# Kernel optimization log

Measured on AMD Instinct MI355X. Metric: run time of the kernel, lower is better.

## Reference

```python
import jax, jax.numpy as jnp
import numpy as np

B, S, D, H, HD = 1, 2048, 1024, 16, 64
WINDOW = 512
RADIUS = max(1, WINDOW // 2)
GLOBAL_IDX = (0, 1, 2, 3)
NEG = -1e9


def rotate_half(x):
    x1, x2 = jnp.split(x, 2, axis=-1)
    return jnp.concatenate([-x2, x1], axis=-1)


def apply_rope(x, cos, sin, pos):
    # x: [b, s, h, hd]; cos/sin: [max_pos, hd]; pos: [b, s]
    c = cos[pos][:, :, None, :]
    s_ = sin[pos][:, :, None, :]
    return x * c + rotate_half(x) * s_


def setup_inputs() -> dict:
    key = jax.random.key(0)
    ks = jax.random.split(key, 12)
    x = jax.random.normal(ks[0], (B, S, D), dtype=jnp.float32)
    # RoPE tables (standard construction)
    inv_freq = 1.0 / (10000.0 ** (jnp.arange(0, HD, 2, dtype=jnp.float32) / HD))
    t = jnp.arange(S, dtype=jnp.float32)
    freqs = jnp.outer(t, inv_freq)                      # [S, HD/2]
    emb = jnp.concatenate([freqs, freqs], axis=-1)      # [S, HD]
    cos_freqs = jnp.cos(emb)
    sin_freqs = jnp.sin(emb)
    position_ids = jnp.broadcast_to(jnp.arange(S, dtype=jnp.int32), (B, S))
    w = lambda k: jax.random.normal(k, (D, D), dtype=jnp.float32) * 0.02
    return {
        "x": x, "cos_freqs": cos_freqs, "sin_freqs": sin_freqs,
        "position_ids": position_ids,
        "Wqs": w(ks[1]), "Wks": w(ks[2]), "Wvs": w(ks[3]),
        "Wqg": w(ks[4]), "Wkg": w(ks[5]), "Wvg": w(ks[6]),
        "Wo": w(ks[7]),
    }


def reference(x, cos_freqs, sin_freqs, position_ids, Wqs, Wks, Wvs, Wqg, Wkg, Wvg, Wo):
    b, s, d = x.shape
    split = lambda y: y.reshape(b, s, H, HD)
    qs = split(x @ Wqs)
    ks_ = split(x @ Wks)
    vs = split(x @ Wvs)
    kg = split(x @ Wkg)
    vg = split(x @ Wvg)
    # (qg projection exists in the module but is unused by its forward math)
    qs = apply_rope(qs, cos_freqs, sin_freqs, position_ids)
    ks_ = apply_rope(ks_, cos_freqs, sin_freqs, position_ids)

    qs_t = jnp.swapaxes(qs, 1, 2)   # [b,h,s,hd]
    ks_t = jnp.swapaxes(ks_, 1, 2)
    vs_t = jnp.swapaxes(vs, 1, 2)
    scale = 1.0 / jnp.sqrt(jnp.float32(HD))

    # local sliding-window (causal) attention over dense scores
    scores = jnp.einsum('bhsd,bhtd->bhst', qs_t, ks_t) * scale
    i = jnp.arange(s)[:, None]
    j = jnp.arange(s)[None, :]
    mask = (jnp.abs(i - j) <= RADIUS) & (j <= i)
    scores = jnp.where(mask[None, None], scores, NEG)
    g = jnp.array(GLOBAL_IDX)
    scores = scores.at[:, :, :, g].add(1e9)  # same as per-index set(score+1e9)
    attn = jax.nn.softmax(scores, axis=-1)
    out_local = jnp.einsum('bhst,bhtd->bhsd', attn, vs_t)
    out_local = jnp.swapaxes(out_local, 1, 2).reshape(b, s, d)

    # global attention: all queries attend to the global-index columns of kg/vg
    kg_t = jnp.swapaxes(kg, 1, 2)
    vg_t = jnp.swapaxes(vg, 1, 2)
    scores_g = jnp.einsum('bhsd,bhtd->bhst', qs_t, kg_t) * scale
    col_mask = jnp.zeros((s,), dtype=bool).at[g].set(True)
    scores_g = jnp.where(col_mask[None, None, None, :], scores_g, NEG)
    attn_g = jax.nn.softmax(scores_g, axis=-1)
    out_global = jnp.einsum('bhst,bhtd->bhsd', attn_g, vg_t)
    out_global = jnp.swapaxes(out_global, 1, 2).reshape(b, s, d)

    return (out_local + out_global) @ Wo
```

## Files before the change

kernel.cpp:

```cpp
#include <hip/hip_runtime.h>

typedef _Float16 half8 __attribute__((ext_vector_type(8)));
typedef float floatx4 __attribute__((ext_vector_type(4)));

#define SEQ 2048
#define DMODEL 1024
#define NHEADS 16
#define HEADDIM 64
#define PW 5120

__global__ __launch_bounds__(256) void k_prep(
    const float* __restrict__ x,
    const float* __restrict__ w0, const float* __restrict__ w1, const float* __restrict__ w2,
    const float* __restrict__ w3, const float* __restrict__ w4, const float* __restrict__ w5,
    _Float16* __restrict__ xh, _Float16* __restrict__ wcat, _Float16* __restrict__ wot) {
  const int tid = threadIdx.x;
  const int b = blockIdx.x;
  if (b < 1024) {
    int base = b * 2048 + tid * 8;
    floatx4 f0 = *(const floatx4*)(x + base);
    floatx4 f1 = *(const floatx4*)(x + base + 4);
    half8 h;
    #pragma unroll
    for (int e = 0; e < 4; ++e) { h[e] = (_Float16)f0[e]; h[e + 4] = (_Float16)f1[e]; }
    *(half8*)(xh + base) = h;
    return;
  }
  __shared__ _Float16 T[64][72];
  int t = b - 1024;
  int z = t >> 8;
  int tile = t & 255;
  int k0 = (tile >> 4) * 64, n0 = (tile & 15) * 64;
  const float* W = (z == 0) ? w0 : (z == 1) ? w1 : (z == 2) ? w2
                 : (z == 3) ? w3 : (z == 4) ? w4 : w5;
  _Float16* dst = (z < 5) ? (wcat + (size_t)z * 1024 * 1024) : wot;

  int lr = tid >> 2, c0 = (tid & 3) * 16;
  #pragma unroll
  for (int i = 0; i < 4; ++i) {
    floatx4 f = *(const floatx4*)(W + (size_t)(k0 + lr) * DMODEL + n0 + c0 + i * 4);
    #pragma unroll
    for (int e = 0; e < 4; ++e) T[c0 + i * 4 + e][lr] = (_Float16)f[e];
  }
  __syncthreads();
  int nr = tid >> 2, s0 = (tid & 3) * 16;
  #pragma unroll
  for (int i = 0; i < 2; ++i) {
    half8 h = *(const half8*)&T[nr][s0 + i * 8];
    *(half8*)(dst + (size_t)(n0 + nr) * DMODEL + k0 + s0 + i * 8) = h;
  }
}

template <bool HALF_OUT, bool FUSE_ROPE, bool SPARSE, int BM, int BN>
__global__ __launch_bounds__(256, 3) void k_gemm(
    const _Float16* __restrict__ A, const _Float16* __restrict__ Bt,
    void* __restrict__ Cv, float* __restrict__ Cp,
    const float* __restrict__ cos_t, const float* __restrict__ sin_t,
    const int* __restrict__ pos, int M, int N, int K) {
  __shared__ _Float16 As[BM][128];
  __shared__ _Float16 Bs[BN][128];
  const int tid = threadIdx.x;
  const int lane = tid & 63;
  const int w = tid >> 6;
  const int l15 = lane & 15;
  const int q4 = lane >> 4;
  constexpr int NJ = (BM == 128) ? 4 : 2;
  const int wm = (BM == 128) ? w * 32 : (w >> 1) * 32;
  const int wn = (BM == 128) ? 0 : (w & 1) * 32;
  int m0, n0;
  if (SPARSE) {
    int b = blockIdx.x;
    if (b < 768) { m0 = (b & 15) * 128; n0 = (b >> 4) * 64; }
    else         { m0 = 0;              n0 = 3072 + (b - 768) * 64; }
  } else {
    m0 = blockIdx.x * BM;
    n0 = blockIdx.y * BN;
  }

  floatx4 acc[2][NJ];
  #pragma unroll
  for (int i = 0; i < 2; ++i)
    #pragma unroll
    for (int j = 0; j < NJ; ++j) acc[i][j] = (floatx4){0.f, 0.f, 0.f, 0.f};

  _Float16* asBase = &As[0][0];
  _Float16* bsBase = &Bs[0][0];
  const int swz = l15 & 7;

  for (int k0 = 0; k0 < K; k0 += 128) {
    __syncthreads();
    #pragma unroll
    for (int it = 0; it < BM / 16; ++it) {
      int c = it * 256 + tid;
      int r = c >> 4, cc = c & 15;
      int g = cc ^ (r & 7);
      __builtin_amdgcn_global_load_lds(
          (const __attribute__((address_space(1))) void*)(A + (size_t)(m0 + r) * K + k0 + g * 8),
          (__attribute__((address_space(3))) void*)(asBase + (it * 256 + w * 64) * 8),
          16, 0, 0);
    }
    #pragma unroll
    for (int it = 0; it < BN / 16; ++it) {
      int c = it * 256 + tid;
      int r = c >> 4, cc = c & 15;
      int g = cc ^ (r & 7);
      __builtin_amdgcn_global_load_lds(
          (const __attribute__((address_space(1))) void*)(Bt + (size_t)(n0 + r) * K + k0 + g * 8),
          (__attribute__((address_space(3))) void*)(bsBase + (it * 256 + w * 64) * 8),
          16, 0, 0);
    }
    __syncthreads();

    #pragma unroll
    for (int kk = 0; kk < 4; ++kk) {
      int q = kk * 4 + q4;
      half8 af[2], bf[NJ];
      #pragma unroll
      for (int t = 0; t < 2; ++t) {
        int ar = wm + t * 16 + l15;
        af[t] = *(const half8*)(asBase + (size_t)ar * 128 + ((q ^ swz) * 8));
      }
      #pragma unroll
      for (int t = 0; t < NJ; ++t) {
        int br = wn + t * 16 + l15;
        bf[t] = *(const half8*)(bsBase + (size_t)br * 128 + ((q ^ swz) * 8));
      }
      #pragma unroll
      for (int i = 0; i < 2; ++i)
        #pragma unroll
        for (int j = 0; j < NJ; ++j)
          acc[i][j] = __builtin_amdgcn_mfma_f32_16x16x32_f16(af[i], bf[j], acc[i][j], 0, 0, 0);
    }
  }

  #pragma unroll
  for (int tm = 0; tm < 2; ++tm) {
    #pragma unroll
    for (int r = 0; r < 4; ++r) {
      int row = m0 + wm + tm * 16 + q4 * 4 + r;
      float v[NJ];
      #pragma unroll
      for (int tn = 0; tn < NJ; ++tn) v[tn] = acc[tm][tn][r];
      if (FUSE_ROPE && NJ == 4 && n0 < 2048) {
        int p = pos[row];
        #pragma unroll
        for (int tn = 0; tn < 2; ++tn) {
          int d = tn * 16 + l15;
          float a = acc[tm][tn][r];
          float bvv = acc[tm][tn + 2][r];
          float c1 = cos_t[p * 64 + d],      s1 = sin_t[p * 64 + d];
          float c2 = cos_t[p * 64 + d + 32], s2 = sin_t[p * 64 + d + 32];
          v[tn]     = a * c1 - bvv * s1;
          v[tn + 2] = bvv * c2 + a * s2;
        }
      }
      #pragma unroll
      for (int tn = 0; tn < NJ; ++tn) {
        int col = n0 + wn + tn * 16 + l15;
        if (HALF_OUT)
          ((_Float16*)Cv)[(size_t)row * N + col] = (_Float16)v[tn];
        else
          Cp[(size_t)row * N + col] = v[tn];
      }
    }
  }
}

__global__ __launch_bounds__(256, 2) void k_attn(const _Float16* __restrict__ proj,
                                                 _Float16* __restrict__ out) {
  const int tid = threadIdx.x;
  const int hb = blockIdx.y * 64;

  if (blockIdx.x >= 28) {
    const int i = (blockIdx.x - 28) * 4 + (tid >> 6);
    const int lane = tid & 63;
    const float scale = 0.125f;
    float qv = (float)proj[(size_t)i * PW + hb + lane];
    float sg[4];
    #pragma unroll
    for (int g = 0; g < 4; ++g) {
      float kgv = (float)proj[(size_t)g * PW + 3072 + hb + lane];
      float v = qv * kgv;
      #pragma unroll
      for (int off = 32; off; off >>= 1) v += __shfl_xor(v, off, 64);
      sg[g] = v * scale;
    }
    float mg = fmaxf(fmaxf(sg[0], sg[1]), fmaxf(sg[2], sg[3]));
    float dg = 0.f, og = 0.f;
    #pragma unroll
    for (int g = 0; g < 4; ++g) {
      float p = __expf(sg[g] - mg);
      dg += p;
      og += p * (float)proj[(size_t)g * PW + 4096 + hb + lane];
    }
    og /= dg;
    int jmin = (i >= 256) ? (i - 256) : 0;
    int jmax = (i < 3) ? i : 3;
    float acc = 0.f;
    for (int j = jmin; j <= jmax; ++j)
      acc += (float)proj[(size_t)j * PW + 2048 + hb + lane];
    float ol = acc / (float)(jmax - jmin + 1);
    out[(size_t)i * DMODEL + hb + lane] = (_Float16)(ol + og);
    return;
  }

  const int i0 = 256 + blockIdx.x * 64;
  const int jlo = i0 - 256;
  const int lane = tid & 63;
  const int w = tid >> 6;
  const int l15 = lane & 15;
  const int q4 = lane >> 4;

  __shared__ _Float16 Qs[64][72];
  __shared__ _Float16 Kc[64][72];
  __shared__ _Float16 Vtc[64][72];
  __shared__ _Float16 Ps[64][72];
  __shared__ _Float16 kg_s[4][64];
  __shared__ _Float16 vg_s[4][64];
  __shared__ float svg_s[64];
  __shared__ float pg_s[4][64];

  #pragma unroll
  for (int rep = 0; rep < 2; ++rep) {
    int c = tid + rep * 256;
    int r = c >> 3, q = c & 7;
    *(half8*)&Qs[r][q * 8] = *(const half8*)(proj + (size_t)(i0 + r) * PW + hb + q * 8);
  }
  {
    int g = tid >> 6, c2 = tid & 63;
    kg_s[g][c2] = proj[(size_t)g * PW + 3072 + hb + c2];
    vg_s[g][c2] = proj[(size_t)g * PW + 4096 + hb + c2];
    if (tid < 64) {
      float s = 0.f;
      #pragma unroll
      for (int g2 = 0; g2 < 4; ++g2) s += (float)proj[(size_t)g2 * PW + 2048 + hb + tid];
      svg_s[tid] = s;
    }
  }
  __syncthreads();

  {
    int ro = w * 16 + (lane >> 2);
    int part = lane & 3;
    float sg[4];
    #pragma unroll
    for (int g = 0; g < 4; ++g) {
      float acc = 0.f;
      #pragma unroll
      for (int u = 0; u < 16; ++u)
        acc += (float)Qs[ro][part * 16 + u] * (float)kg_s[g][part * 16 + u];
      acc += __shfl_xor(acc, 1, 64);
      acc += __shfl_xor(acc, 2, 64);
      sg[g] = acc * 0.125f;
    }
    float mg = fmaxf(fmaxf(sg[0], sg[1]), fmaxf(sg[2], sg[3]));
    float dg = 0.f;
    #pragma unroll
    for (int g = 0; g < 4; ++g) dg += __expf(sg[g] - mg);
    pg_s[part][ro] = __expf(sg[part] - mg) / dg;
  }

  half8 qf0 = *(const half8*)&Qs[w * 16 + l15][q4 * 8];
  half8 qf1 = *(const half8*)&Qs[w * 16 + l15][32 + q4 * 8];

  float lpart[4];
  floatx4 oacc[4];
  #pragma unroll
  for (int cb = 0; cb < 4; ++cb) {
    oacc[cb] = (floatx4){0.f, 0.f, 0.f, 0.f};
    lpart[cb] = 0.f;
  }

  const int kr_r0 = tid >> 3, kr_q = tid & 7;
  const int kr_r1 = kr_r0 + 32;
  const int vj0 = (tid & 7) + ((tid >> 6) << 3);
  const int vj1 = vj0 + 32;
  const int vd0 = ((tid >> 3) & 7) * 8;

  half8 kr0, kr1, vr0, vr1;
  {
    const _Float16* kb = proj + (size_t)jlo * PW + 1024 + hb;
    const _Float16* vb = proj + (size_t)jlo * PW + 2048 + hb;
    kr0 = *(const half8*)(kb + (size_t)kr_r0 * PW + kr_q * 8);
    kr1 = *(const half8*)(kb + (size_t)kr_r1 * PW + kr_q * 8);
    vr0 = *(const half8*)(vb + (size_t)vj0 * PW + vd0);
    vr1 = *(const half8*)(vb + (size_t)vj1 * PW + vd0);
  }

  for (int cc = 0; cc < 5; ++cc) {
    __syncthreads();
    *(half8*)&Kc[kr_r0][kr_q * 8] = kr0;
    *(half8*)&Kc[kr_r1][kr_q * 8] = kr1;
    #pragma unroll
    for (int u = 0; u < 8; ++u) {
      int d = vd0 + u;
      Vtc[d][vj0 ^ (d & 56)] = vr0[u];
      Vtc[d][vj1 ^ (d & 56)] = vr1[u];
    }
    if (cc < 4) {
      const _Float16* kb = proj + (size_t)(jlo + (cc + 1) * 64) * PW + 1024 + hb;
      const _Float16* vb = proj + (size_t)(jlo + (cc + 1) * 64) * PW + 2048 + hb;
      kr0 = *(const half8*)(kb + (size_t)kr_r0 * PW + kr_q * 8);
      kr1 = *(const half8*)(kb + (size_t)kr_r1 * PW + kr_q * 8);
      vr0 = *(const half8*)(vb + (size_t)vj0 * PW + vd0);
      vr1 = *(const half8*)(vb + (size_t)vj1 * PW + vd0);
    }
    __syncthreads();

    float sc[4][4];
    #pragma unroll
    for (int cb = 0; cb < 4; ++cb) {
      half8 b0 = *(const half8*)&Kc[cb * 16 + l15][q4 * 8];
      half8 b1 = *(const half8*)&Kc[cb * 16 + l15][32 + q4 * 8];
      floatx4 a = (floatx4){0.f, 0.f, 0.f, 0.f};
      a = __builtin_amdgcn_mfma_f32_16x16x32_f16(qf0, b0, a, 0, 0, 0);
      a = __builtin_amdgcn_mfma_f32_16x16x32_f16(qf1, b1, a, 0, 0, 0);
      #pragma unroll
      for (int r = 0; r < 4; ++r) sc[cb][r] = a[r];
    }

    #pragma unroll
    for (int r = 0; r < 4; ++r) {
      int ri = w * 16 + q4 * 4 + r;
      float rowp = 0.f;
      #pragma unroll
      for (int cb = 0; cb < 4; ++cb) {
        int jjg = cc * 64 + cb * 16 + l15;
        bool valid = (jjg >= ri) && (jjg <= ri + 256);
        float p = valid ? __expf(sc[cb][r] * 0.125f) : 0.f;
        Ps[ri][cb * 16 + l15] = (_Float16)p;
        rowp += p;
      }
      lpart[r] += rowp;
    }

    half8 pf0 = *(const half8*)&Ps[w * 16 + l15][q4 * 8];
    half8 pf1 = *(const half8*)&Ps[w * 16 + l15][32 + q4 * 8];
    #pragma unroll
    for (int cb = 0; cb < 4; ++cb) {
      int dv = cb * 16 + l15;
      half8 v0 = *(const half8*)&Vtc[dv][(q4 * 8) ^ (dv & 56)];
      half8 v1 = *(const half8*)&Vtc[dv][(32 + q4 * 8) ^ (dv & 56)];
      oacc[cb] = __builtin_amdgcn_mfma_f32_16x16x32_f16(pf0, v0, oacc[cb], 0, 0, 0);
      oacc[cb] = __builtin_amdgcn_mfma_f32_16x16x32_f16(pf1, v1, oacc[cb], 0, 0, 0);
    }
  }

  #pragma unroll
  for (int r = 0; r < 4; ++r) {
    int ri = w * 16 + q4 * 4 + r;
    if (i0 + ri < 260) continue;
    float lsum = lpart[r];
    #pragma unroll
    for (int off = 1; off < 16; off <<= 1) lsum += __shfl_xor(lsum, off, 64);
    float inv = 1.f / (lsum + 4.f);
    #pragma unroll
    for (int cb = 0; cb < 4; ++cb) {
      int col = cb * 16 + l15;
      float ol = (oacc[cb][r] + svg_s[col]) * inv;
      float og = 0.f;
      #pragma unroll
      for (int g = 0; g < 4; ++g) og += pg_s[g][ri] * (float)vg_s[g][col];
      out[(size_t)(i0 + ri) * DMODEL + hb + col] = (_Float16)(ol + og);
    }
  }
}

extern "C" void kernel_launch(void* const* d_in, const int* in_sizes, int n_in,
                              void* d_out, int out_size, void* d_ws, size_t ws_size,
                              hipStream_t stream) {
  const float* x     = (const float*)d_in[0];
  const float* cos_t = (const float*)d_in[1];
  const float* sin_t = (const float*)d_in[2];
  const int*   pos   = (const int*)d_in[3];
  const float* Wqs   = (const float*)d_in[4];
  const float* Wks   = (const float*)d_in[5];
  const float* Wvs   = (const float*)d_in[6];
  const float* Wkg   = (const float*)d_in[8];
  const float* Wvg   = (const float*)d_in[9];
  const float* Wo    = (const float*)d_in[10];
  float* out = (float*)d_out;

  char* ws = (char*)d_ws;
  _Float16* xh   = (_Float16*)(ws);
  _Float16* wcat = (_Float16*)(ws + (4u << 20));
  _Float16* wot  = (_Float16*)(ws + (14u << 20));
  _Float16* proj = (_Float16*)(ws + (16u << 20));
  _Float16* attn = (_Float16*)(ws + (36u << 20));

  k_prep<<<2560, 256, 0, stream>>>(x, Wqs, Wks, Wvs, Wkg, Wvg, Wo, xh, wcat, wot);
  k_gemm<true, true, true, 128, 64><<<800, 256, 0, stream>>>(
      xh, wcat, proj, nullptr, cos_t, sin_t, pos, SEQ, PW, DMODEL);
  k_attn<<<dim3(93, NHEADS), 256, 0, stream>>>(proj, attn);
  k_gemm<false, false, false, 64, 64><<<dim3(32, 16), 256, 0, stream>>>(
      attn, wot, nullptr, out, cos_t, sin_t, pos, SEQ, DMODEL, DMODEL);
}
```

Baseline: 153.7 us.

## Halve attention query tile to 32 rows and swizzle GEMM block order

The attention kernel now processes 32 query rows per block with 128 threads instead of 64 rows with 256 threads. This doubles the grid so more blocks are spread across CUs, but each block reloads the same 320-row K/V window, so K/V traffic per query roughly doubles. Both GEMM launches also remap block indices with an XCD-style interleave (b&7 major) so neighbouring tiles land on the same chiplet and share L2. The output GEMM moves to a 1D grid to support this remapping.

```diff
diff --git a/kernel.cpp b/kernel.cpp
--- a/kernel.cpp
+++ b/kernel.cpp
@@ -70,11 +70,14 @@
   int m0, n0;
   if (SPARSE) {
     int b = blockIdx.x;
+    b = (b & 7) * 100 + (b >> 3);
     if (b < 768) { m0 = (b & 15) * 128; n0 = (b >> 4) * 64; }
     else         { m0 = 0;              n0 = 3072 + (b - 768) * 64; }
   } else {
-    m0 = blockIdx.x * BM;
-    n0 = blockIdx.y * BN;
+    int b = blockIdx.x;
+    b = (b & 7) * 64 + (b >> 3);
+    m0 = (b & 31) * BM;
+    n0 = (b >> 5) * BN;
   }
 
   floatx4 acc[2][NJ];
@@ -166,13 +169,13 @@
   }
 }
 
-__global__ __launch_bounds__(256, 2) void k_attn(const _Float16* __restrict__ proj,
+__global__ __launch_bounds__(128, 2) void k_attn(const _Float16* __restrict__ proj,
                                                  _Float16* __restrict__ out) {
   const int tid = threadIdx.x;
   const int hb = blockIdx.y * 64;
 
-  if (blockIdx.x >= 28) {
-    const int i = (blockIdx.x - 28) * 4 + (tid >> 6);
+  if (blockIdx.x >= 56) {
+    const int i = (blockIdx.x - 56) * 2 + (tid >> 6);
     const int lane = tid & 63;
     const float scale = 0.125f;
     float qv = (float)proj[(size_t)i * PW + hb + lane];
@@ -204,38 +207,40 @@
     return;
   }
 
-  const int i0 = 256 + blockIdx.x * 64;
+  const int i0 = 256 + blockIdx.x * 32;
   const int jlo = i0 - 256;
   const int lane = tid & 63;
   const int w = tid >> 6;
   const int l15 = lane & 15;
   const int q4 = lane >> 4;
 
-  __shared__ _Float16 Qs[64][72];
+  __shared__ _Float16 Qs[32][72];
   __shared__ _Float16 Kc[64][72];
   __shared__ _Float16 Vtc[64][72];
-  __shared__ _Float16 Ps[64][72];
+  __shared__ _Float16 Ps[32][72];
   __shared__ _Float16 kg_s[4][64];
   __shared__ _Float16 vg_s[4][64];
   __shared__ float svg_s[64];
-  __shared__ float pg_s[4][64];
+  __shared__ float pg_s[4][32];
 
   #pragma unroll
   for (int rep = 0; rep < 2; ++rep) {
-    int c = tid + rep * 256;
+    int c = tid + rep * 128;
     int r = c >> 3, q = c & 7;
     *(half8*)&Qs[r][q * 8] = *(const half8*)(proj + (size_t)(i0 + r) * PW + hb + q * 8);
   }
-  {
-    int g = tid >> 6, c2 = tid & 63;
+  #pragma unroll
+  for (int rep = 0; rep < 2; ++rep) {
+    int idx = tid + rep * 128;
+    int g = idx >> 6, c2 = idx & 63;
     kg_s[g][c2] = proj[(size_t)g * PW + 3072 + hb + c2];
     vg_s[g][c2] = proj[(size_t)g * PW + 4096 + hb + c2];
-    if (tid < 64) {
-      float s = 0.f;
-      #pragma unroll
-      for (int g2 = 0; g2 < 4; ++g2) s += (float)proj[(size_t)g2 * PW + 2048 + hb + tid];
-      svg_s[tid] = s;
-    }
+  }
+  if (tid < 64) {
+    float s = 0.f;
+    #pragma unroll
+    for (int g2 = 0; g2 < 4; ++g2) s += (float)proj[(size_t)g2 * PW + 2048 + hb + tid];
+    svg_s[tid] = s;
   }
   __syncthreads();
 
@@ -271,39 +276,40 @@
     lpart[cb] = 0.f;
   }
 
-  const int kr_r0 = tid >> 3, kr_q = tid & 7;
-  const int kr_r1 = kr_r0 + 32;
-  const int vj0 = (tid & 7) + ((tid >> 6) << 3);
-  const int vj1 = vj0 + 32;
+  const int krr = tid >> 3, krq = tid & 7;
+  const int vjb = (tid & 7) + ((tid >> 6) << 3);
   const int vd0 = ((tid >> 3) & 7) * 8;
 
-  half8 kr0, kr1, vr0, vr1;
+  half8 kr[4], vr[4];
   {
     const _Float16* kb = proj + (size_t)jlo * PW + 1024 + hb;
     const _Float16* vb = proj + (size_t)jlo * PW + 2048 + hb;
-    kr0 = *(const half8*)(kb + (size_t)kr_r0 * PW + kr_q * 8);
-    kr1 = *(const half8*)(kb + (size_t)kr_r1 * PW + kr_q * 8);
-    vr0 = *(const half8*)(vb + (size_t)vj0 * PW + vd0);
-    vr1 = *(const half8*)(vb + (size_t)vj1 * PW + vd0);
+    #pragma unroll
+    for (int it = 0; it < 4; ++it) {
+      kr[it] = *(const half8*)(kb + (size_t)(krr + it * 16) * PW + krq * 8);
+      vr[it] = *(const half8*)(vb + (size_t)(vjb + it * 16) * PW + vd0);
+    }
   }
 
   for (int cc = 0; cc < 5; ++cc) {
     __syncthreads();
-    *(half8*)&Kc[kr_r0][kr_q * 8] = kr0;
-    *(half8*)&Kc[kr_r1][kr_q * 8] = kr1;
-    #pragma unroll
-    for (int u = 0; u < 8; ++u) {
-      int d = vd0 + u;
-      Vtc[d][vj0 ^ (d & 56)] = vr0[u];
-      Vtc[d][vj1 ^ (d & 56)] = vr1[u];
+    #pragma unroll
+    for (int it = 0; it < 4; ++it) {
+      *(half8*)&Kc[krr + it * 16][krq * 8] = kr[it];
+      #pragma unroll
+      for (int u = 0; u < 8; ++u) {
+        int d = vd0 + u;
+        Vtc[d][(vjb + it * 16) ^ (d & 56)] = vr[it][u];
+      }
     }
     if (cc < 4) {
       const _Float16* kb = proj + (size_t)(jlo + (cc + 1) * 64) * PW + 1024 + hb;
       const _Float16* vb = proj + (size_t)(jlo + (cc + 1) * 64) * PW + 2048 + hb;
-      kr0 = *(const half8*)(kb + (size_t)kr_r0 * PW + kr_q * 8);
-      kr1 = *(const half8*)(kb + (size_t)kr_r1 * PW + kr_q * 8);
-      vr0 = *(const half8*)(vb + (size_t)vj0 * PW + vd0);
-      vr1 = *(const half8*)(vb + (size_t)vj1 * PW + vd0);
+      #pragma unroll
+      for (int it = 0; it < 4; ++it) {
+        kr[it] = *(const half8*)(kb + (size_t)(krr + it * 16) * PW + krq * 8);
+        vr[it] = *(const half8*)(vb + (size_t)(vjb + it * 16) * PW + vd0);
+      }
     }
     __syncthreads();
 
@@ -391,7 +397,7 @@
   k_prep<<<2560, 256, 0, stream>>>(x, Wqs, Wks, Wvs, Wkg, Wvg, Wo, xh, wcat, wot);
   k_gemm<true, true, true, 128, 64><<<800, 256, 0, stream>>>(
       xh, wcat, proj, nullptr, cos_t, sin_t, pos, SEQ, PW, DMODEL);
-  k_attn<<<dim3(93, NHEADS), 256, 0, stream>>>(proj, attn);
-  k_gemm<false, false, false, 64, 64><<<dim3(32, 16), 256, 0, stream>>>(
+  k_attn<<<dim3(186, NHEADS), 128, 0, stream>>>(proj, attn);
+  k_gemm<false, false, false, 64, 64><<<512, 256, 0, stream>>>(
       attn, wot, nullptr, out, cos_t, sin_t, pos, SEQ, DMODEL, DMODEL);
 }
```

New measurement: 159.8 us. 3.9% more time.
